# Kernel tuning notes

Measured on AMD Instinct MI355X. Metric: run time of the kernel, lower is better.

The kernel has to match this reference:

```python
import jax, jax.numpy as jnp
import numpy as np

NV = 6890   # SMPL vertex count (hard-coded in module)
NF = 13776  # SMPL face count
BATCH = 64


def _make_laplacian():
    # Mirrors LaplacianLoss.__init__: symmetric -1 adjacency from triangle
    # faces, diagonal = vertex degree, each row normalized by diag + 1e-8.
    rng = np.random.default_rng(0)
    faces = rng.integers(0, NV, size=(NF, 3))
    L = np.zeros((NV, NV), dtype=np.float32)
    L[faces[:, 0], faces[:, 1]] = -1
    L[faces[:, 1], faces[:, 0]] = -1
    L[faces[:, 1], faces[:, 2]] = -1
    L[faces[:, 2], faces[:, 1]] = -1
    L[faces[:, 2], faces[:, 0]] = -1
    L[faces[:, 0], faces[:, 2]] = -1
    r, c = np.diag_indices(NV)
    L[r, c] = -L.sum(1)
    L = L / (np.diag(L)[:, None] + 1e-8)
    return jnp.asarray(L)


def setup_inputs() -> dict:
    key = jax.random.key(0)
    x = jax.random.normal(key, (BATCH, NV, 3), dtype=jnp.float32)
    laplacian = _make_laplacian()
    return {"x": x, "laplacian": laplacian}


def reference(x, laplacian):
    # Dense Laplacian applied per batch: [v,w] x [b,w,d] -> [b,v,d]
    lx = jnp.einsum('vw,bwd->bvd', laplacian, x)
    # Squared norm over coordinate dim, then mean over (batch, vertices)
    # (average=False branch of the original module).
    return jnp.mean(jnp.sum(lx * lx, axis=2))
```

## Files before the change

### kernel.cpp

```cpp
#include <hip/hip_runtime.h>

#define NV    6890
#define NB    64
#define NCOL  192
#define NC4   48
#define MAIN4 1722
#define NITP  32
#define DEPTH 8
#define VCAP  128
#define SCALE (1.0f / (64.0f * 6890.0f))

__global__ __launch_bounds__(256) void transpose_x_kernel(
    const float* __restrict__ x, float* __restrict__ Xt) {
  int i = blockIdx.x * blockDim.x + threadIdx.x;
  const int total = NV * NCOL;
  if (i >= total) return;
  int n = i % NCOL;
  int w = i / NCOL;
  Xt[i] = x[(size_t)(n / 3) * (NV * 3) + (size_t)w * 3 + (n % 3)];
}

template <bool USE_PARTIALS>
__global__ __launch_bounds__(128) void lap_rows_wave_kernel(
    const float* __restrict__ L,
    const float* __restrict__ Xt,
    float* __restrict__ partials,
    float* __restrict__ out_atomic) {
  const int lane = threadIdx.x & 63;
  const int wv   = threadIdx.x >> 6;
  const int v    = blockIdx.x * 2 + wv;
  if (v >= NV) return;

  __shared__ float4 s_c4[2][VCAP];
  __shared__ int    s_cb[2][VCAP];
  float4* __restrict__ sc4 = s_c4[wv];
  int*    __restrict__ scb = s_cb[wv];

  const float* __restrict__ row = L + (size_t)v * NV;
  const int head     = (v & 1) ? 2 : 0;
  const int extraPos = head ? 0 : (NV - 2);
  const float4* __restrict__ m4 = (const float4*)(row + head);
  const unsigned long long lmask = (1ull << lane) - 1ull;

  int nnz = 0;

  auto pushc = [&](unsigned long long m, float4 f, int colbase) {
    if (m) {
      const int pos = nnz + __popcll(m & lmask);
      const bool mine = (m >> lane) & 1ull;
      if (mine && pos < VCAP) { sc4[pos] = f; scb[pos] = colbase; }
      nnz += __popcll(m);
    }
  };

  {
    const float h0 = row[extraPos];
    const float h1 = row[extraPos + 1];
    const bool nz = (lane == 0) &&
                    ((__float_as_uint(h0) | __float_as_uint(h1)) != 0u);
    pushc(__ballot(nz), make_float4(h0, h1, 0.f, 0.f), extraPos);
  }

  float4 buf[DEPTH];
  #pragma unroll
  for (int k = 0; k < DEPTH; ++k) buf[k] = m4[k * 64 + lane];

  #pragma unroll DEPTH
  for (int it = 0; it < NITP; ++it) {
    const float4 f = buf[it & (DEPTH - 1)];
    buf[it & (DEPTH - 1)] = m4[min((it + DEPTH) * 64 + lane, MAIN4 - 1)];
    const int i = it * 64 + lane;
    const unsigned u = __float_as_uint(f.x) | __float_as_uint(f.y) |
                       __float_as_uint(f.z) | __float_as_uint(f.w);
    pushc(__ballot((i < MAIN4) && (u != 0u)), f, head + i * 4);
  }

  float4 acc = make_float4(0.f, 0.f, 0.f, 0.f);

  auto gatherc = [&](float val, int col) {
    if (lane < NC4) {
      const float4 g = ((const float4*)Xt)[(size_t)col * NC4 + lane];
      acc.x = fmaf(val, g.x, acc.x);
      acc.y = fmaf(val, g.y, acc.y);
      acc.z = fmaf(val, g.z, acc.z);
      acc.w = fmaf(val, g.w, acc.w);
    }
  };

  if (nnz <= VCAP) {
    const int cnt = nnz;
    for (int j = 0; j < cnt; ++j) {
      const float4 c = sc4[j];
      const int   cb = scb[j];
      if (__float_as_uint(c.x)) gatherc(c.x, cb);
      if (__float_as_uint(c.y)) gatherc(c.y, cb + 1);
      if (__float_as_uint(c.z)) gatherc(c.z, cb + 2);
      if (__float_as_uint(c.w)) gatherc(c.w, cb + 3);
    }
  } else {
    acc = make_float4(0.f, 0.f, 0.f, 0.f);
    auto walk = [&](unsigned long long m, float src, int col0, int stride) {
      while (m) {
        const int s = (int)__builtin_ctzll(m);
        m &= m - 1;
        const float val =
            __int_as_float(__builtin_amdgcn_readlane(__float_as_int(src), s));
        gatherc(val, col0 + s * stride);
      }
    };
    {
      const bool act = lane < 2;
      const float val = act ? row[extraPos + lane] : 0.f;
      walk(__ballot(act && val != 0.f), val, extraPos, 1);
    }
    for (int it = 0; it < 27; ++it) {
      const int i = it * 64 + lane;
      const bool act = i < MAIN4;
      float4 f = make_float4(0.f, 0.f, 0.f, 0.f);
      if (act) f = m4[i];
      const int cb = head + it * 256;
      walk(__ballot(act && f.x != 0.f), f.x, cb + 0, 4);
      walk(__ballot(act && f.y != 0.f), f.y, cb + 1, 4);
      walk(__ballot(act && f.z != 0.f), f.z, cb + 2, 4);
      walk(__ballot(act && f.w != 0.f), f.w, cb + 3, 4);
    }
  }

  float sq = fmaf(acc.x, acc.x,
             fmaf(acc.y, acc.y,
             fmaf(acc.z, acc.z, acc.w * acc.w)));
  #pragma unroll
  for (int o = 32; o > 0; o >>= 1) sq += __shfl_down(sq, o);
  if (lane == 0) {
    if (USE_PARTIALS) partials[v] = sq;
    else              atomicAdd(out_atomic, sq * SCALE);
  }
}

template <bool USE_PARTIALS>
__global__ __launch_bounds__(256) void lap_fused_kernel(
    const float* __restrict__ L, const float* __restrict__ x,
    float* __restrict__ partials, float* __restrict__ out_atomic) {
  const int lane = threadIdx.x & 63;
  const int wv   = threadIdx.x >> 6;
  const int v    = blockIdx.x * 4 + wv;
  if (v >= NV) return;

  const float* __restrict__ row = L + (size_t)v * NV;
  const int head     = (v & 1) ? 2 : 0;
  const int extraPos = head ? 0 : (NV - 2);
  const float4* __restrict__ m4 = (const float4*)(row + head);

  const int n0 = lane, n1 = lane + 64, n2 = lane + 128;
  const int o0 = (n0 / 3) * (NV * 3) + (n0 % 3);
  const int o1 = (n1 / 3) * (NV * 3) + (n1 % 3);
  const int o2 = (n2 / 3) * (NV * 3) + (n2 % 3);

  float a0 = 0.f, a1 = 0.f, a2 = 0.f;
  auto walk = [&](unsigned long long m, float src, int col0, int stride) {
    while (m) {
      const int s = (int)__builtin_ctzll(m);
      m &= m - 1;
      const float val =
          __int_as_float(__builtin_amdgcn_readlane(__float_as_int(src), s));
      const int cb = (col0 + s * stride) * 3;
      a0 = fmaf(val, x[cb + o0], a0);
      a1 = fmaf(val, x[cb + o1], a1);
      a2 = fmaf(val, x[cb + o2], a2);
    }
  };
  {
    const bool act = lane < 2;
    const float val = act ? row[extraPos + lane] : 0.f;
    walk(__ballot(act && val != 0.f), val, extraPos, 1);
  }
  for (int it = 0; it < 27; ++it) {
    const int i = it * 64 + lane;
    const bool act = i < MAIN4;
    float4 f = make_float4(0.f, 0.f, 0.f, 0.f);
    if (act) f = m4[i];
    const int cb = head + it * 256;
    walk(__ballot(act && f.x != 0.f), f.x, cb + 0, 4);
    walk(__ballot(act && f.y != 0.f), f.y, cb + 1, 4);
    walk(__ballot(act && f.z != 0.f), f.z, cb + 2, 4);
    walk(__ballot(act && f.w != 0.f), f.w, cb + 3, 4);
  }

  float sq = fmaf(a0, a0, fmaf(a1, a1, a2 * a2));
  #pragma unroll
  for (int o = 32; o > 0; o >>= 1) sq += __shfl_down(sq, o);
  if (lane == 0) {
    if (USE_PARTIALS) partials[v] = sq;
    else              atomicAdd(out_atomic, sq * SCALE);
  }
}

__global__ __launch_bounds__(256) void reduce_kernel(
    const float* __restrict__ p, float* __restrict__ out) {
  int tid = threadIdx.x;
  float a = 0.0f;
  for (int i = tid; i < NV; i += 256) a += p[i];
  #pragma unroll
  for (int o = 32; o > 0; o >>= 1) a += __shfl_down(a, o);
  __shared__ float s_w[4];
  if ((tid & 63) == 0) s_w[tid >> 6] = a;
  __syncthreads();
  if (tid == 0) out[0] = (s_w[0] + s_w[1] + s_w[2] + s_w[3]) * SCALE;
}

__global__ void zero_out_kernel(float* p) {
  if (threadIdx.x == 0 && blockIdx.x == 0) p[0] = 0.0f;
}

extern "C" void kernel_launch(void* const* d_in, const int* in_sizes, int n_in,
                              void* d_out, int out_size, void* d_ws, size_t ws_size,
                              hipStream_t stream) {
  const float* x = (const float*)d_in[0];
  const float* L = (const float*)d_in[1];
  float* out = (float*)d_out;

  const size_t xt_bytes   = (size_t)NV * NCOL * sizeof(float);
  const size_t part_bytes = (size_t)NV * sizeof(float);

  if (ws_size >= xt_bytes + part_bytes) {
    float* Xt       = (float*)d_ws;
    float* partials = (float*)((char*)d_ws + xt_bytes);
    const int total = NV * NCOL;
    transpose_x_kernel<<<(total + 255) / 256, 256, 0, stream>>>(x, Xt);
    lap_rows_wave_kernel<true><<<(NV + 1) / 2, 128, 0, stream>>>(L, Xt, partials, nullptr);
    reduce_kernel<<<1, 256, 0, stream>>>(partials, out);
  } else if (ws_size >= part_bytes) {
    float* partials = (float*)d_ws;
    lap_fused_kernel<true><<<(NV + 3) / 4, 256, 0, stream>>>(L, x, partials, nullptr);
    reduce_kernel<<<1, 256, 0, stream>>>(partials, out);
  } else {
    zero_out_kernel<<<1, 64, 0, stream>>>(out);
    lap_fused_kernel<false><<<(NV + 3) / 4, 256, 0, stream>>>(L, x, nullptr, out);
  }
}
```

Baseline: 60.95 us.

## Split row compression and sparse gather into separate kernels via global workspace

Splits the fused per-row kernel into a compress kernel, which scans each dense Laplacian row and writes up to 32 nonzero float4 chunks plus column indices to global workspace, and an SpMM kernel that reads those entries and gathers from transposed x. Both kernels now run 4 waves per block and no longer use shared-memory staging, so the dense scan and the gather can each run at their own occupancy. The cost is an extra launch and a global write/read of the compressed entries. The dense 190 MB row scan still happens every call, so the change mainly reshapes the schedule rather than removing work.

Measured after the change: 72.62 us. 1.19x slower.

```diff
diff --git a/kernel.cpp b/kernel.cpp
--- a/kernel.cpp
+++ b/kernel.cpp
@@ -1,13 +1,11 @@
 #include <hip/hip_runtime.h>
 
 #define NV    6890
-#define NB    64
 #define NCOL  192
 #define NC4   48
 #define MAIN4 1722
 #define NITP  32
-#define DEPTH 8
-#define VCAP  128
+#define CCAP  32
 #define SCALE (1.0f / (64.0f * 6890.0f))
 
 __global__ __launch_bounds__(256) void transpose_x_kernel(
@@ -20,35 +18,28 @@
   Xt[i] = x[(size_t)(n / 3) * (NV * 3) + (size_t)w * 3 + (n % 3)];
 }
 
-template <bool USE_PARTIALS>
-__global__ __launch_bounds__(128) void lap_rows_wave_kernel(
-    const float* __restrict__ L,
-    const float* __restrict__ Xt,
-    float* __restrict__ partials,
-    float* __restrict__ out_atomic) {
+__global__ __launch_bounds__(256) void compress_kernel(
+    const float* __restrict__ L, float4* __restrict__ ent4,
+    int* __restrict__ entc, int* __restrict__ cnt) {
   const int lane = threadIdx.x & 63;
   const int wv   = threadIdx.x >> 6;
-  const int v    = blockIdx.x * 2 + wv;
+  const int v    = blockIdx.x * 4 + wv;
   if (v >= NV) return;
-
-  __shared__ float4 s_c4[2][VCAP];
-  __shared__ int    s_cb[2][VCAP];
-  float4* __restrict__ sc4 = s_c4[wv];
-  int*    __restrict__ scb = s_cb[wv];
 
   const float* __restrict__ row = L + (size_t)v * NV;
   const int head     = (v & 1) ? 2 : 0;
   const int extraPos = head ? 0 : (NV - 2);
   const float4* __restrict__ m4 = (const float4*)(row + head);
   const unsigned long long lmask = (1ull << lane) - 1ull;
+  float4* __restrict__ re4 = ent4 + (size_t)v * CCAP;
+  int*    __restrict__ rec = entc + (size_t)v * CCAP;
 
   int nnz = 0;
-
   auto pushc = [&](unsigned long long m, float4 f, int colbase) {
     if (m) {
       const int pos = nnz + __popcll(m & lmask);
       const bool mine = (m >> lane) & 1ull;
-      if (mine && pos < VCAP) { sc4[pos] = f; scb[pos] = colbase; }
+      if (mine && pos < CCAP) { re4[pos] = f; rec[pos] = colbase; }
       nnz += __popcll(m);
     }
   };
@@ -61,22 +52,34 @@
     pushc(__ballot(nz), make_float4(h0, h1, 0.f, 0.f), extraPos);
   }
 
-  float4 buf[DEPTH];
-  #pragma unroll
-  for (int k = 0; k < DEPTH; ++k) buf[k] = m4[k * 64 + lane];
-
-  #pragma unroll DEPTH
+  float4 buf[8];
+  #pragma unroll
+  for (int k = 0; k < 8; ++k) buf[k] = m4[k * 64 + lane];
+
+  #pragma unroll 8
   for (int it = 0; it < NITP; ++it) {
-    const float4 f = buf[it & (DEPTH - 1)];
-    buf[it & (DEPTH - 1)] = m4[min((it + DEPTH) * 64 + lane, MAIN4 - 1)];
+    const float4 f = buf[it & 7];
+    buf[it & 7] = m4[min((it + 8) * 64 + lane, MAIN4 - 1)];
     const int i = it * 64 + lane;
     const unsigned u = __float_as_uint(f.x) | __float_as_uint(f.y) |
                        __float_as_uint(f.z) | __float_as_uint(f.w);
     pushc(__ballot((i < MAIN4) && (u != 0u)), f, head + i * 4);
   }
+  if (lane == 0) cnt[v] = nnz;
+}
+
+template <bool USE_PARTIALS>
+__global__ __launch_bounds__(256) void spmm_xt_kernel(
+    const float* __restrict__ L, const float* __restrict__ Xt,
+    const float4* __restrict__ ent4, const int* __restrict__ entc,
+    const int* __restrict__ cnt, float* __restrict__ partials,
+    float* __restrict__ out_atomic) {
+  const int lane = threadIdx.x & 63;
+  const int wv   = threadIdx.x >> 6;
+  const int v    = blockIdx.x * 4 + wv;
+  if (v >= NV) return;
 
   float4 acc = make_float4(0.f, 0.f, 0.f, 0.f);
-
   auto gatherc = [&](float val, int col) {
     if (lane < NC4) {
       const float4 g = ((const float4*)Xt)[(size_t)col * NC4 + lane];
@@ -87,18 +90,23 @@
     }
   };
 
-  if (nnz <= VCAP) {
-    const int cnt = nnz;
-    for (int j = 0; j < cnt; ++j) {
-      const float4 c = sc4[j];
-      const int   cb = scb[j];
-      if (__float_as_uint(c.x)) gatherc(c.x, cb);
-      if (__float_as_uint(c.y)) gatherc(c.y, cb + 1);
-      if (__float_as_uint(c.z)) gatherc(c.z, cb + 2);
-      if (__float_as_uint(c.w)) gatherc(c.w, cb + 3);
+  const int c = cnt[v];
+  if (c <= CCAP) {
+    const float4* __restrict__ re4 = ent4 + (size_t)v * CCAP;
+    const int*    __restrict__ rec = entc + (size_t)v * CCAP;
+    for (int j = 0; j < c; ++j) {
+      const float4 f = re4[j];
+      const int   cb = rec[j];
+      if (__float_as_uint(f.x)) gatherc(f.x, cb);
+      if (__float_as_uint(f.y)) gatherc(f.y, cb + 1);
+      if (__float_as_uint(f.z)) gatherc(f.z, cb + 2);
+      if (__float_as_uint(f.w)) gatherc(f.w, cb + 3);
     }
   } else {
-    acc = make_float4(0.f, 0.f, 0.f, 0.f);
+    const float* __restrict__ row = L + (size_t)v * NV;
+    const int head     = (v & 1) ? 2 : 0;
+    const int extraPos = head ? 0 : (NV - 2);
+    const float4* __restrict__ m4 = (const float4*)(row + head);
     auto walk = [&](unsigned long long m, float src, int col0, int stride) {
       while (m) {
         const int s = (int)__builtin_ctzll(m);
@@ -220,21 +228,31 @@
   float* out = (float*)d_out;
 
   const size_t xt_bytes   = (size_t)NV * NCOL * sizeof(float);
+  const size_t e4_bytes   = (size_t)NV * CCAP * sizeof(float4);
+  const size_t ec_bytes   = (size_t)NV * CCAP * sizeof(int);
+  const size_t cnt_bytes  = (size_t)NV * sizeof(int);
   const size_t part_bytes = (size_t)NV * sizeof(float);
-
-  if (ws_size >= xt_bytes + part_bytes) {
-    float* Xt       = (float*)d_ws;
-    float* partials = (float*)((char*)d_ws + xt_bytes);
-    const int total = NV * NCOL;
-    transpose_x_kernel<<<(total + 255) / 256, 256, 0, stream>>>(x, Xt);
-    lap_rows_wave_kernel<true><<<(NV + 1) / 2, 128, 0, stream>>>(L, Xt, partials, nullptr);
+  const int grid = (NV + 3) / 4;
+
+  if (ws_size >= xt_bytes + e4_bytes + ec_bytes + cnt_bytes + part_bytes) {
+    char* p = (char*)d_ws;
+    float*  Xt       = (float*)p;              p += xt_bytes;
+    float4* ent4     = (float4*)p;             p += e4_bytes;
+    int*    entc     = (int*)p;                p += ec_bytes;
+    int*    cnt      = (int*)p;                p += cnt_bytes;
+    float*  partials = (float*)p;
+
+    compress_kernel<<<grid, 256, 0, stream>>>(L, ent4, entc, cnt);
+    transpose_x_kernel<<<(NV * NCOL + 255) / 256, 256, 0, stream>>>(x, Xt);
+    spmm_xt_kernel<true><<<grid, 256, 0, stream>>>(L, Xt, ent4, entc, cnt,
+                                                   partials, nullptr);
     reduce_kernel<<<1, 256, 0, stream>>>(partials, out);
   } else if (ws_size >= part_bytes) {
     float* partials = (float*)d_ws;
-    lap_fused_kernel<true><<<(NV + 3) / 4, 256, 0, stream>>>(L, x, partials, nullptr);
+    lap_fused_kernel<true><<<grid, 256, 0, stream>>>(L, x, partials, nullptr);
     reduce_kernel<<<1, 256, 0, stream>>>(partials, out);
   } else {
     zero_out_kernel<<<1, 64, 0, stream>>>(out);
-    lap_fused_kernel<false><<<(NV + 3) / 4, 256, 0, stream>>>(L, x, nullptr, out);
-  }
-}
+    lap_fused_kernel<false><<<grid, 256, 0, stream>>>(L, x, nullptr, out);
+  }
+}
```

## Build global nonzero bitmap of L in a streaming scan fused with transpose

Applied to the files above, without the earlier changes.

Replaces the per-row wave compaction with a separate streaming pass that scans the whole Laplacian as flat float4s and writes a 64-bit ballot mask per 64 float4s, fused into the same launch as the x transpose. The apply kernel then reads only the bitmap words covering its row and fetches the nonzero float4s before gathering from transposed x. The intent is a fully coalesced, row-alignment-free scan of the dense matrix and a cheaper sparse apply, at the cost of an extra bitmap buffer in workspace and a second, scattered read of the nonzero L entries.

New measurement: 73.42 us. 20.5% more time.

```diff
diff --git a/kernel.cpp b/kernel.cpp
--- a/kernel.cpp
+++ b/kernel.cpp
@@ -1,85 +1,82 @@
 #include <hip/hip_runtime.h>
 
-#define NV    6890
-#define NB    64
-#define NCOL  192
-#define NC4   48
-#define MAIN4 1722
-#define NITP  32
-#define DEPTH 8
-#define VCAP  128
-#define SCALE (1.0f / (64.0f * 6890.0f))
-
-__global__ __launch_bounds__(256) void transpose_x_kernel(
-    const float* __restrict__ x, float* __restrict__ Xt) {
-  int i = blockIdx.x * blockDim.x + threadIdx.x;
-  const int total = NV * NCOL;
-  if (i >= total) return;
-  int n = i % NCOL;
-  int w = i / NCOL;
-  Xt[i] = x[(size_t)(n / 3) * (NV * 3) + (size_t)w * 3 + (n % 3)];
-}
-
-template <bool USE_PARTIALS>
-__global__ __launch_bounds__(128) void lap_rows_wave_kernel(
-    const float* __restrict__ L,
-    const float* __restrict__ Xt,
-    float* __restrict__ partials,
-    float* __restrict__ out_atomic) {
+#define NV     6890
+#define NCOL   192
+#define NC4    48
+#define NELEM  47472100
+#define C4TOT  11868025
+#define NWORDS 185438
+#define SCANB  2048
+#define SCANW  8192
+#define FULLIT 22
+#define TRANB  5168
+#define MAIN4  1722
+#define SCALE  (1.0f / (64.0f * 6890.0f))
+
+__global__ __launch_bounds__(256) void scan_transpose_kernel(
+    const float* __restrict__ L, const float* __restrict__ x,
+    float* __restrict__ Xt, unsigned long long* __restrict__ bm) {
+  if (blockIdx.x < SCANB) {
+    const int lane = threadIdx.x & 63;
+    const int w    = blockIdx.x * 4 + (threadIdx.x >> 6);
+    const float4* __restrict__ Lf4 = (const float4*)L;
+
+    #pragma unroll 8
+    for (int it = 0; it < FULLIT; ++it) {
+      const int s = w + it * SCANW;
+      const float4 f = Lf4[(size_t)s * 64 + lane];
+      const unsigned u = __float_as_uint(f.x) | __float_as_uint(f.y) |
+                         __float_as_uint(f.z) | __float_as_uint(f.w);
+      const unsigned long long m = __ballot(u != 0u);
+      if (lane == 0) bm[s] = m;
+    }
+    {
+      const int s = w + FULLIT * SCANW;
+      if (s < NWORDS) {
+        const int c = s * 64 + lane;
+        float4 f = make_float4(0.f, 0.f, 0.f, 0.f);
+        if (c < C4TOT) f = Lf4[c];
+        const unsigned u = __float_as_uint(f.x) | __float_as_uint(f.y) |
+                           __float_as_uint(f.z) | __float_as_uint(f.w);
+        const unsigned long long m = __ballot(u != 0u);
+        if (lane == 0) bm[s] = m;
+      }
+    }
+  } else {
+    const int t = (blockIdx.x - SCANB) * 256 + threadIdx.x;
+    if (t < NV * NCOL) {
+      const int n = t % NCOL;
+      const int w = t / NCOL;
+      Xt[t] = x[(size_t)(n / 3) * (NV * 3) + (size_t)w * 3 + (n % 3)];
+    }
+  }
+}
+
+__global__ __launch_bounds__(256) void apply_kernel(
+    const float* __restrict__ L, const float* __restrict__ Xt,
+    const unsigned long long* __restrict__ bm, float* __restrict__ partials) {
   const int lane = threadIdx.x & 63;
   const int wv   = threadIdx.x >> 6;
-  const int v    = blockIdx.x * 2 + wv;
+  const int v    = blockIdx.x * 4 + wv;
   if (v >= NV) return;
 
-  __shared__ float4 s_c4[2][VCAP];
-  __shared__ int    s_cb[2][VCAP];
-  float4* __restrict__ sc4 = s_c4[wv];
-  int*    __restrict__ scb = s_cb[wv];
-
-  const float* __restrict__ row = L + (size_t)v * NV;
-  const int head     = (v & 1) ? 2 : 0;
-  const int extraPos = head ? 0 : (NV - 2);
-  const float4* __restrict__ m4 = (const float4*)(row + head);
-  const unsigned long long lmask = (1ull << lane) - 1ull;
-
-  int nnz = 0;
-
-  auto pushc = [&](unsigned long long m, float4 f, int colbase) {
-    if (m) {
-      const int pos = nnz + __popcll(m & lmask);
-      const bool mine = (m >> lane) & 1ull;
-      if (mine && pos < VCAP) { sc4[pos] = f; scb[pos] = colbase; }
-      nnz += __popcll(m);
-    }
-  };
-
-  {
-    const float h0 = row[extraPos];
-    const float h1 = row[extraPos + 1];
-    const bool nz = (lane == 0) &&
-                    ((__float_as_uint(h0) | __float_as_uint(h1)) != 0u);
-    pushc(__ballot(nz), make_float4(h0, h1, 0.f, 0.f), extraPos);
-  }
-
-  float4 buf[DEPTH];
-  #pragma unroll
-  for (int k = 0; k < DEPTH; ++k) buf[k] = m4[k * 64 + lane];
-
-  #pragma unroll DEPTH
-  for (int it = 0; it < NITP; ++it) {
-    const float4 f = buf[it & (DEPTH - 1)];
-    buf[it & (DEPTH - 1)] = m4[min((it + DEPTH) * 64 + lane, MAIN4 - 1)];
-    const int i = it * 64 + lane;
-    const unsigned u = __float_as_uint(f.x) | __float_as_uint(f.y) |
-                       __float_as_uint(f.z) | __float_as_uint(f.w);
-    pushc(__ballot((i < MAIN4) && (u != 0u)), f, head + i * 4);
-  }
-
+  const int rbase  = v * NV;
+  const int rend   = rbase + NV;
+  const int cfirst = rbase >> 2;
+  const int clast  = (rend - 1) >> 2;
+  const int w0     = cfirst >> 6;
+  const int nw     = (clast >> 6) - w0 + 1;
+
+  const unsigned long long myw =
+      (lane < nw) ? bm[w0 + lane] : 0ull;
+
+  const float4* __restrict__ Lf4 = (const float4*)L;
+  const float4* __restrict__ Xt4 = (const float4*)Xt;
   float4 acc = make_float4(0.f, 0.f, 0.f, 0.f);
 
   auto gatherc = [&](float val, int col) {
     if (lane < NC4) {
-      const float4 g = ((const float4*)Xt)[(size_t)col * NC4 + lane];
+      const float4 g = Xt4[(size_t)col * NC4 + lane];
       acc.x = fmaf(val, g.x, acc.x);
       acc.y = fmaf(val, g.y, acc.y);
       acc.z = fmaf(val, g.z, acc.z);
@@ -87,42 +84,24 @@
     }
   };
 
-  if (nnz <= VCAP) {
-    const int cnt = nnz;
-    for (int j = 0; j < cnt; ++j) {
-      const float4 c = sc4[j];
-      const int   cb = scb[j];
-      if (__float_as_uint(c.x)) gatherc(c.x, cb);
-      if (__float_as_uint(c.y)) gatherc(c.y, cb + 1);
-      if (__float_as_uint(c.z)) gatherc(c.z, cb + 2);
-      if (__float_as_uint(c.w)) gatherc(c.w, cb + 3);
-    }
-  } else {
-    acc = make_float4(0.f, 0.f, 0.f, 0.f);
-    auto walk = [&](unsigned long long m, float src, int col0, int stride) {
-      while (m) {
-        const int s = (int)__builtin_ctzll(m);
-        m &= m - 1;
-        const float val =
-            __int_as_float(__builtin_amdgcn_readlane(__float_as_int(src), s));
-        gatherc(val, col0 + s * stride);
-      }
-    };
-    {
-      const bool act = lane < 2;
-      const float val = act ? row[extraPos + lane] : 0.f;
-      walk(__ballot(act && val != 0.f), val, extraPos, 1);
-    }
-    for (int it = 0; it < 27; ++it) {
-      const int i = it * 64 + lane;
-      const bool act = i < MAIN4;
-      float4 f = make_float4(0.f, 0.f, 0.f, 0.f);
-      if (act) f = m4[i];
-      const int cb = head + it * 256;
-      walk(__ballot(act && f.x != 0.f), f.x, cb + 0, 4);
-      walk(__ballot(act && f.y != 0.f), f.y, cb + 1, 4);
-      walk(__ballot(act && f.z != 0.f), f.z, cb + 2, 4);
-      walk(__ballot(act && f.w != 0.f), f.w, cb + 3, 4);
+  for (int j = 0; j < nw; ++j) {
+    unsigned long long word = __shfl(myw, j);
+    const int lo = (j == 0) ? (cfirst & 63) : 0;
+    const int hi = (j == nw - 1) ? (clast & 63) : 63;
+    word &= (~0ull >> (63 - hi)) & (~0ull << lo);
+    while (word) {
+      const int s = (int)__builtin_ctzll(word);
+      word &= word - 1;
+      const int c = (w0 + j) * 64 + s;
+      const float4 f = Lf4[c];
+      const int e0 = c * 4;
+      if (e0 >= rbase && e0 < rend && __float_as_uint(f.x)) gatherc(f.x, e0 - rbase);
+      const int e1 = e0 + 1;
+      if (e1 >= rbase && e1 < rend && __float_as_uint(f.y)) gatherc(f.y, e1 - rbase);
+      const int e2 = e0 + 2;
+      if (e2 >= rbase && e2 < rend && __float_as_uint(f.z)) gatherc(f.z, e2 - rbase);
+      const int e3 = e0 + 3;
+      if (e3 >= rbase && e3 < rend && __float_as_uint(f.w)) gatherc(f.w, e3 - rbase);
     }
   }
 
@@ -131,10 +110,7 @@
              fmaf(acc.z, acc.z, acc.w * acc.w)));
   #pragma unroll
   for (int o = 32; o > 0; o >>= 1) sq += __shfl_down(sq, o);
-  if (lane == 0) {
-    if (USE_PARTIALS) partials[v] = sq;
-    else              atomicAdd(out_atomic, sq * SCALE);
-  }
+  if (lane == 0) partials[v] = sq;
 }
 
 template <bool USE_PARTIALS>
@@ -220,14 +196,17 @@
   float* out = (float*)d_out;
 
   const size_t xt_bytes   = (size_t)NV * NCOL * sizeof(float);
+  const size_t bm_bytes   = ((size_t)NWORDS * 8 + 255) & ~(size_t)255;
   const size_t part_bytes = (size_t)NV * sizeof(float);
 
-  if (ws_size >= xt_bytes + part_bytes) {
-    float* Xt       = (float*)d_ws;
-    float* partials = (float*)((char*)d_ws + xt_bytes);
-    const int total = NV * NCOL;
-    transpose_x_kernel<<<(total + 255) / 256, 256, 0, stream>>>(x, Xt);
-    lap_rows_wave_kernel<true><<<(NV + 1) / 2, 128, 0, stream>>>(L, Xt, partials, nullptr);
+  if (ws_size >= xt_bytes + bm_bytes + part_bytes) {
+    char* p = (char*)d_ws;
+    float*              Xt       = (float*)p;               p += xt_bytes;
+    unsigned long long* bm       = (unsigned long long*)p;  p += bm_bytes;
+    float*              partials = (float*)p;
+
+    scan_transpose_kernel<<<SCANB + TRANB, 256, 0, stream>>>(L, x, Xt, bm);
+    apply_kernel<<<(NV + 3) / 4, 256, 0, stream>>>(L, Xt, bm, partials);
     reduce_kernel<<<1, 256, 0, stream>>>(partials, out);
   } else if (ws_size >= part_bytes) {
     float* partials = (float*)d_ws;
```
